# Performance work log

Hardware: AMD Instinct MI355X
Metric: run time of the kernel (lower is better)

Reference implementation:

```python
import jax, jax.numpy as jnp
import numpy as np

HEADS = 16
DIM_HEAD = 64
SCALE = DIM_HEAD ** -0.5
NEG = -jnp.finfo(jnp.float32).max


def setup_inputs() -> dict:
    key = jax.random.key(0)
    k1, k2, k3, k4, k5 = jax.random.split(key, 5)
    dim = 1024
    inner = HEADS * DIM_HEAD
    b, n = 2, 2048
    s = dim ** -0.5
    return {
        "x": jax.random.normal(k1, (b, n, dim), dtype=jnp.float32),
        "Wq": jax.random.normal(k2, (dim, inner), dtype=jnp.float32) * s,
        "Wk": jax.random.normal(k3, (dim, inner), dtype=jnp.float32) * s,
        "Wv": jax.random.normal(k4, (dim, inner), dtype=jnp.float32) * s,
        "Wo": jax.random.normal(k5, (inner, dim), dtype=jnp.float32) * s,
    }


def reference(x, Wq, Wk, Wv, Wo):
    b, n, _ = x.shape
    # project and split heads: b n (h d) -> b h n d
    def split(t):
        return t.reshape(b, n, HEADS, DIM_HEAD).transpose(0, 2, 1, 3)
    q = split(x @ Wq) * SCALE
    k = split(x @ Wk)
    v = split(x @ Wv)
    sim = jnp.einsum('bhid,bhjd->bhij', q, k)
    # causal mask: triu(j - i + 1) masked with -finfo.max
    causal = jnp.triu(jnp.ones((n, n), dtype=bool), k=1)
    sim = jnp.where(causal, NEG, sim)
    attn = jax.nn.softmax(sim, axis=-1)  # dropout p=0.0 -> identity
    out = jnp.einsum('bhij,bhjd->bhid', attn, v)
    out = out.transpose(0, 2, 1, 3).reshape(b, n, HEADS * DIM_HEAD)
    return out @ Wo
```

## Files before the change

### kernel.cpp

```cpp
#include <hip/hip_runtime.h>

#define NHEAD 16
#define DHEAD 64
#define SEQ 2048
#define DMODEL 1024
#define BATCH 2
#define QSCALE 0.1803368801111204f

typedef __bf16 bf16x8 __attribute__((ext_vector_type(8)));
typedef float f32x4 __attribute__((ext_vector_type(4)));
typedef float f32x16 __attribute__((ext_vector_type(16)));
typedef unsigned int u32x4 __attribute__((ext_vector_type(4)));

__device__ inline unsigned short f2bf(float f) {
  unsigned int u = __builtin_bit_cast(unsigned int, f);
  u = (u + 0x7FFFu + ((u >> 16) & 1u)) >> 16;
  return (unsigned short)u;
}

__device__ inline unsigned int cvtpk_bf16(float lo, float hi) {
  unsigned int r;
  asm("v_cvt_pk_bf16_f32 %0, %1, %2" : "=v"(r) : "v"(lo), "v"(hi));
  return r;
}

__device__ inline void pl32swap(unsigned int& a, unsigned int& b) {
  asm volatile("v_permlane32_swap_b32 %0, %1" : "+v"(a), "+v"(b));
}

__global__ __launch_bounds__(256) void k_conv_x(const float* __restrict__ x,
                                                unsigned short* __restrict__ Af) {
  int blk = blockIdx.x;
  int R = blk >> 5, kt = blk & 31;
  int t = threadIdx.x;
  int i = t >> 6, lane = t & 63;
  int n = R * 64 + i * 16 + (lane & 15);
  int k = kt * 32 + (lane >> 4) * 8;
  const float* xp = x + (size_t)n * DMODEL + k;
  float4 v0 = *(const float4*)xp;
  float4 v1 = *(const float4*)(xp + 4);
  ushort4 lo, hi;
  lo.x = f2bf(v0.x); lo.y = f2bf(v0.y); lo.z = f2bf(v0.z); lo.w = f2bf(v0.w);
  hi.x = f2bf(v1.x); hi.y = f2bf(v1.y); hi.z = f2bf(v1.z); hi.w = f2bf(v1.w);
  size_t base = ((size_t)((R * 32 + kt) * 4 + i) * 64 + lane) * 8;
  *(ushort4*)&Af[base] = lo;
  *(ushort4*)&Af[base + 4] = hi;
}

__global__ __launch_bounds__(256) void k_trans_wf(const float* __restrict__ Wq, const float* __restrict__ Wk,
                                                  const float* __restrict__ Wv, const float* __restrict__ Wo,
                                                  unsigned short* __restrict__ Wqf, unsigned short* __restrict__ Wkf,
                                                  unsigned short* __restrict__ Wvf, unsigned short* __restrict__ Wof) {
  __shared__ float ts[32][65];
  int mat = blockIdx.z;
  const float* src = (mat == 0) ? Wq : (mat == 1) ? Wk : (mat == 2) ? Wv : Wo;
  unsigned short* dst = (mat == 0) ? Wqf : (mat == 1) ? Wkf : (mat == 2) ? Wvf : Wof;
  int cb = blockIdx.x, kt = blockIdx.y;
  int t = threadIdx.x;
  int row = t >> 3, seg = t & 7;
  const float* sp = src + (size_t)(kt * 32 + row) * DMODEL + cb * 64 + seg * 8;
  float4 u0 = *(const float4*)sp;
  float4 u1 = *(const float4*)(sp + 4);
  ts[row][seg * 8 + 0] = u0.x; ts[row][seg * 8 + 1] = u0.y;
  ts[row][seg * 8 + 2] = u0.z; ts[row][seg * 8 + 3] = u0.w;
  ts[row][seg * 8 + 4] = u1.x; ts[row][seg * 8 + 5] = u1.y;
  ts[row][seg * 8 + 6] = u1.z; ts[row][seg * 8 + 7] = u1.w;
  __syncthreads();
  int j = t >> 6, lane = t & 63;
  int c_l = j * 16 + (lane & 15);
  int kb = (lane >> 4) * 8;
  ushort4 lo, hi;
  lo.x = f2bf(ts[kb + 0][c_l]); lo.y = f2bf(ts[kb + 1][c_l]);
  lo.z = f2bf(ts[kb + 2][c_l]); lo.w = f2bf(ts[kb + 3][c_l]);
  hi.x = f2bf(ts[kb + 4][c_l]); hi.y = f2bf(ts[kb + 5][c_l]);
  hi.z = f2bf(ts[kb + 6][c_l]); hi.w = f2bf(ts[kb + 7][c_l]);
  size_t base = ((size_t)((cb * 32 + kt) * 4 + j) * 64 + lane) * 8;
  *(ushort4*)&dst[base] = lo;
  *(ushort4*)&dst[base + 4] = hi;
}

__global__ __launch_bounds__(128, 2) void k_gemm_qkv(const unsigned short* __restrict__ Af,
                                                     const unsigned short* __restrict__ Wqf,
                                                     const unsigned short* __restrict__ Wkf,
                                                     const unsigned short* __restrict__ Wvf,
                                                     unsigned short* __restrict__ Qf,
                                                     unsigned short* __restrict__ Kf,
                                                     unsigned short* __restrict__ Vf) {
  int id = blockIdx.x;
  int xcd = id & 7, lid = id >> 3;
  int rq = lid / 12, cw = lid % 12;
  int rho = (xcd >> 1) * 8 + rq;
  int wv = threadIdx.x >> 6;
  int R = rho * 2 + wv;
  int ct = (xcd & 1) * 12 + cw;
  int mat = ct >> 3, cb2 = ct & 7;
  const unsigned short* Bf = (mat == 0) ? Wqf : (mat == 1) ? Wkf : Wvf;
  int lane = threadIdx.x & 63;
  const unsigned short* Ap  = Af + (size_t)R * 65536 + lane * 8;
  const unsigned short* Bp0 = Bf + (size_t)(cb2 * 2) * 65536 + lane * 8;
  const unsigned short* Bp1 = Bp0 + 65536;

  f32x4 acc[4][8] = {};
  bf16x8 a0[4], a1[4], b0[8], b1[8];
#pragma unroll
  for (int i = 0; i < 4; i++) a0[i] = *(const bf16x8*)(Ap + i * 512);
#pragma unroll
  for (int j = 0; j < 4; j++) {
    b0[j]     = *(const bf16x8*)(Bp0 + j * 512);
    b0[4 + j] = *(const bf16x8*)(Bp1 + j * 512);
  }
#pragma unroll 1
  for (int kt = 0; kt < 32; kt += 2) {
    {
      const unsigned short* An = Ap + (kt + 1) * 2048;
      const unsigned short* Bn0 = Bp0 + (kt + 1) * 2048;
      const unsigned short* Bn1 = Bp1 + (kt + 1) * 2048;
#pragma unroll
      for (int i = 0; i < 4; i++) a1[i] = *(const bf16x8*)(An + i * 512);
#pragma unroll
      for (int j = 0; j < 4; j++) {
        b1[j]     = *(const bf16x8*)(Bn0 + j * 512);
        b1[4 + j] = *(const bf16x8*)(Bn1 + j * 512);
      }
    }
#pragma unroll
    for (int i = 0; i < 4; i++)
#pragma unroll
      for (int j = 0; j < 8; j++)
        acc[i][j] = __builtin_amdgcn_mfma_f32_16x16x32_bf16(a0[i], b0[j], acc[i][j], 0, 0, 0);
    if (kt + 2 < 32) {
      const unsigned short* An = Ap + (kt + 2) * 2048;
      const unsigned short* Bn0 = Bp0 + (kt + 2) * 2048;
      const unsigned short* Bn1 = Bp1 + (kt + 2) * 2048;
#pragma unroll
      for (int i = 0; i < 4; i++) a0[i] = *(const bf16x8*)(An + i * 512);
#pragma unroll
      for (int j = 0; j < 4; j++) {
        b0[j]     = *(const bf16x8*)(Bn0 + j * 512);
        b0[4 + j] = *(const bf16x8*)(Bn1 + j * 512);
      }
    }
#pragma unroll
    for (int i = 0; i < 4; i++)
#pragma unroll
      for (int j = 0; j < 8; j++)
        acc[i][j] = __builtin_amdgcn_mfma_f32_16x16x32_bf16(a1[i], b1[j], acc[i][j], 0, 0, 0);
  }

#pragma unroll
  for (int i = 0; i < 4; i++)
#pragma unroll
    for (int j = 0; j < 8; j++) {
      int n_g = R * 64 + i * 16 + ((lane >> 4) << 2);
      int c = cb2 * 128 + j * 16 + (lane & 15);
      int b = n_g >> 11, n0 = n_g & 2047;
      int h = c >> 6, d = c & 63;
      int bh = b * NHEAD + h;
      if (mat == 0) {
        size_t base = ((size_t)(bh * 64 + (n0 >> 5)) * 4 + (d >> 4)) * 512 +
                      (size_t)((((d >> 3) & 1) * 32 + (n0 & 31)) * 8 + (d & 7));
#pragma unroll
        for (int r = 0; r < 4; r++) Qf[base + 8 * r] = f2bf(acc[i][j][r] * QSCALE);
      } else if (mat == 1) {
        size_t base = ((size_t)(bh * 32 + (n0 >> 6)) * 8 + ((d >> 4) + 4 * ((n0 >> 5) & 1))) * 512 +
                      (size_t)((((d >> 3) & 1) * 32 + (n0 & 31)) * 8 + (d & 7));
#pragma unroll
        for (int r = 0; r < 4; r++) Kf[base + 8 * r] = f2bf(acc[i][j][r]);
      } else {
        size_t base = ((size_t)(bh * 32 + (n0 >> 6)) * 8 + (((n0 >> 4) & 3) + 4 * (d >> 5))) * 512 +
                      (size_t)((((n0 >> 3) & 1) * 32 + (d & 31)) * 8 + (n0 & 7));
        ushort4 o;
        o.x = f2bf(acc[i][j][0]); o.y = f2bf(acc[i][j][1]);
        o.z = f2bf(acc[i][j][2]); o.w = f2bf(acc[i][j][3]);
        *(ushort4*)&Vf[base] = o;
      }
    }
}

__global__ __launch_bounds__(64, 2) void k_attn(const unsigned short* __restrict__ Qf,
                                                const unsigned short* __restrict__ Kf,
                                                const unsigned short* __restrict__ Vf,
                                                unsigned short* __restrict__ Obf) {
  int id = blockIdx.x;
  int xcd = id & 7, m = id >> 3;
  int bhl = m & 3, u = m >> 2;
  int bh = xcd * 4 + bhl;
  int v = (u < 32) ? (63 - u) : (u - 32);
  int nk = (v >> 1) + 1;
  int lane = threadIdx.x;
  int h = lane >> 5, ql = lane & 31;
  int qrow = v * 32 + ql;

  const unsigned short* Qp = Qf + (size_t)bh * 131072 + (size_t)v * 2048;
  const unsigned short* Kp = Kf + (size_t)bh * 131072;
  const unsigned short* Vp = Vf + (size_t)bh * 131072;
  int b = bh >> 4, hh = bh & 15;

  bf16x8 qv[4];
#pragma unroll
  for (int ds = 0; ds < 4; ds++)
    qv[ds] = *(const bf16x8*)&Qp[ds * 512 + lane * 8];

  bf16x8 Kr[8], Vr[8];
#pragma unroll
  for (int jj = 0; jj < 8; jj++) Kr[jj] = *(const bf16x8*)&Kp[jj * 512 + lane * 8];
#pragma unroll
  for (int jj = 0; jj < 8; jj++) Vr[jj] = *(const bf16x8*)&Vp[jj * 512 + lane * 8];

  f32x16 o0 = {}, o1 = {};
  float m_r = -3.0e38f, l_r = 0.0f;

#pragma unroll 1
  for (int kc = 0; kc < nk; ++kc) {
    f32x16 s0 = {}, s1 = {};
#pragma unroll
    for (int ds = 0; ds < 4; ds++) {
      s0 = __builtin_amdgcn_mfma_f32_32x32x16_bf16(Kr[ds], qv[ds], s0, 0, 0, 0);
      s1 = __builtin_amdgcn_mfma_f32_32x32x16_bf16(Kr[4 + ds], qv[ds], s1, 0, 0, 0);
    }
    bool pfn = (kc + 1 < nk);
    size_t nb = (size_t)(kc + 1) * 4096;
    if (pfn) {
#pragma unroll
      for (int jj = 0; jj < 8; jj++) Kr[jj] = *(const bf16x8*)&Kp[nb + jj * 512 + lane * 8];
    }
    int k0 = kc * 64;
    if (kc == nk - 1) {
#pragma unroll
      for (int r = 0; r < 16; r++) {
        int kloc = (r & 3) + 8 * (r >> 2) + 4 * h;
        if (k0 + kloc > qrow) s0[r] = -3.0e38f;
        if (k0 + 32 + kloc > qrow) s1[r] = -3.0e38f;
      }
    }
    float t0[8], t1[8];
#pragma unroll
    for (int r = 0; r < 8; r++) t0[r] = fmaxf(s0[r], s0[r + 8]);
#pragma unroll
    for (int r = 0; r < 8; r++) t1[r] = fmaxf(s1[r], s1[r + 8]);
#pragma unroll
    for (int r = 0; r < 4; r++) t0[r] = fmaxf(fmaxf(t0[r], t0[r + 4]), fmaxf(t1[r], t1[r + 4]));
    float pm = fmaxf(fmaxf(t0[0], t0[1]), fmaxf(t0[2], t0[3]));
    pm = fmaxf(pm, __shfl_xor(pm, 32));
    bool grow = pm > m_r + 8.0f;
    float mnew = grow ? pm : m_r;
    float sf = grow ? __builtin_amdgcn_exp2f(m_r - mnew) : 1.0f;
    m_r = mnew;
    float rsum = 0.0f;
#pragma unroll
    for (int r = 0; r < 16; r++) { s0[r] = __builtin_amdgcn_exp2f(s0[r] - m_r); rsum += s0[r]; }
#pragma unroll
    for (int r = 0; r < 16; r++) { s1[r] = __builtin_amdgcn_exp2f(s1[r] - m_r); rsum += s1[r]; }
    l_r = l_r * sf + rsum;
    if (__ballot(grow)) {
#pragma unroll
      for (int r = 0; r < 16; r++) { o0[r] *= sf; o1[r] *= sf; }
    }
    unsigned int pa0 = cvtpk_bf16(s0[0], s0[1]),   pa1 = cvtpk_bf16(s0[2], s0[3]);
    unsigned int pb0 = cvtpk_bf16(s0[4], s0[5]),   pb1 = cvtpk_bf16(s0[6], s0[7]);
    unsigned int pc0 = cvtpk_bf16(s0[8], s0[9]),   pc1 = cvtpk_bf16(s0[10], s0[11]);
    unsigned int pd0 = cvtpk_bf16(s0[12], s0[13]), pd1 = cvtpk_bf16(s0[14], s0[15]);
    unsigned int pe0 = cvtpk_bf16(s1[0], s1[1]),   pe1 = cvtpk_bf16(s1[2], s1[3]);
    unsigned int pf0 = cvtpk_bf16(s1[4], s1[5]),   pf1 = cvtpk_bf16(s1[6], s1[7]);
    unsigned int pg0 = cvtpk_bf16(s1[8], s1[9]),   pg1 = cvtpk_bf16(s1[10], s1[11]);
    unsigned int ph0 = cvtpk_bf16(s1[12], s1[13]), ph1 = cvtpk_bf16(s1[14], s1[15]);
    pl32swap(pa0, pb0); pl32swap(pa1, pb1);
    pl32swap(pc0, pd0); pl32swap(pc1, pd1);
    pl32swap(pe0, pf0); pl32swap(pe1, pf1);
    pl32swap(pg0, ph0); pl32swap(pg1, ph1);
    bf16x8 pfr[4];
    pfr[0] = __builtin_bit_cast(bf16x8, (u32x4){pa0, pa1, pb0, pb1});
    pfr[1] = __builtin_bit_cast(bf16x8, (u32x4){pc0, pc1, pd0, pd1});
    pfr[2] = __builtin_bit_cast(bf16x8, (u32x4){pe0, pe1, pf0, pf1});
    pfr[3] = __builtin_bit_cast(bf16x8, (u32x4){pg0, pg1, ph0, ph1});
#pragma unroll
    for (int ks = 0; ks < 4; ks++) {
      o0 = __builtin_amdgcn_mfma_f32_32x32x16_bf16(Vr[ks], pfr[ks], o0, 0, 0, 0);
      o1 = __builtin_amdgcn_mfma_f32_32x32x16_bf16(Vr[4 + ks], pfr[ks], o1, 0, 0, 0);
    }
    if (pfn) {
#pragma unroll
      for (int jj = 0; jj < 8; jj++) Vr[jj] = *(const bf16x8*)&Vp[nb + jj * 512 + lane * 8];
    }
  }

  float lt = l_r + __shfl_xor(l_r, 32);
  float rl = 1.0f / lt;
  int Rg = b * 32 + (v >> 1);
  int ii = (v * 2 + (ql >> 4)) & 3;
  size_t base0 = ((size_t)(Rg * 32 + 2 * hh) * 4 + ii) * 512 + (size_t)((ql & 15) * 8 + 4 * h);
  size_t base1 = base0 + 2048;
#pragma unroll
  for (int rg = 0; rg < 4; rg++) {
    uint2 w0, w1;
    w0.x = cvtpk_bf16(o0[4 * rg] * rl, o0[4 * rg + 1] * rl);
    w0.y = cvtpk_bf16(o0[4 * rg + 2] * rl, o0[4 * rg + 3] * rl);
    w1.x = cvtpk_bf16(o1[4 * rg] * rl, o1[4 * rg + 1] * rl);
    w1.y = cvtpk_bf16(o1[4 * rg + 2] * rl, o1[4 * rg + 3] * rl);
    *(uint2*)&Obf[base0 + rg * 128] = w0;
    *(uint2*)&Obf[base1 + rg * 128] = w1;
  }
}

__global__ __launch_bounds__(64, 2) void k_gemm_out(const unsigned short* __restrict__ Obf,
                                                    const unsigned short* __restrict__ Wof,
                                                    float* __restrict__ out) {
  int id = blockIdx.x;
  int xcd = id & 7, lid = id >> 3;
  int rg8 = lid >> 4, cb = lid & 15;
  int R = xcd * 8 + rg8;
  int lane = threadIdx.x;
  const unsigned short* Ap = Obf + (size_t)R * 65536 + lane * 8;
  const unsigned short* Bp = Wof + (size_t)cb * 65536 + lane * 8;

  f32x4 acc[4][4] = {};
  bf16x8 a0[4], b0[4], a1[4], b1[4];
#pragma unroll
  for (int i = 0; i < 4; i++) {
    a0[i] = *(const bf16x8*)(Ap + i * 512);
    b0[i] = *(const bf16x8*)(Bp + i * 512);
  }
#pragma unroll 1
  for (int kt = 0; kt < 32; kt += 2) {
    {
      const unsigned short* An = Ap + (kt + 1) * 2048;
      const unsigned short* Bn = Bp + (kt + 1) * 2048;
#pragma unroll
      for (int i = 0; i < 4; i++) {
        a1[i] = *(const bf16x8*)(An + i * 512);
        b1[i] = *(const bf16x8*)(Bn + i * 512);
      }
    }
#pragma unroll
    for (int i = 0; i < 4; i++)
#pragma unroll
      for (int j = 0; j < 4; j++)
        acc[i][j] = __builtin_amdgcn_mfma_f32_16x16x32_bf16(a0[i], b0[j], acc[i][j], 0, 0, 0);
    if (kt + 2 < 32) {
      const unsigned short* An = Ap + (kt + 2) * 2048;
      const unsigned short* Bn = Bp + (kt + 2) * 2048;
#pragma unroll
      for (int i = 0; i < 4; i++) {
        a0[i] = *(const bf16x8*)(An + i * 512);
        b0[i] = *(const bf16x8*)(Bn + i * 512);
      }
    }
#pragma unroll
    for (int i = 0; i < 4; i++)
#pragma unroll
      for (int j = 0; j < 4; j++)
        acc[i][j] = __builtin_amdgcn_mfma_f32_16x16x32_bf16(a1[i], b1[j], acc[i][j], 0, 0, 0);
  }

#pragma unroll
  for (int i = 0; i < 4; i++)
#pragma unroll
    for (int j = 0; j < 4; j++) {
      int n_g = R * 64 + i * 16 + ((lane >> 4) << 2);
      int c = cb * 64 + j * 16 + (lane & 15);
#pragma unroll
      for (int r = 0; r < 4; r++)
        out[(size_t)(n_g + r) * DMODEL + c] = acc[i][j][r];
    }
}

extern "C" void kernel_launch(void* const* d_in, const int* in_sizes, int n_in,
                              void* d_out, int out_size, void* d_ws, size_t ws_size,
                              hipStream_t stream) {
  const float* x  = (const float*)d_in[0];
  const float* Wq = (const float*)d_in[1];
  const float* Wk = (const float*)d_in[2];
  const float* Wv = (const float*)d_in[3];
  const float* Wo = (const float*)d_in[4];
  float* out = (float*)d_out;
  char* ws = (char*)d_ws;
  unsigned short* Af  = (unsigned short*)(ws);
  unsigned short* Wqf = (unsigned short*)(ws + (8ull << 20));
  unsigned short* Wkf = (unsigned short*)(ws + (10ull << 20));
  unsigned short* Wvf = (unsigned short*)(ws + (12ull << 20));
  unsigned short* Wof = (unsigned short*)(ws + (14ull << 20));
  unsigned short* Qf  = (unsigned short*)(ws + (16ull << 20));
  unsigned short* Kf  = (unsigned short*)(ws + (24ull << 20));
  unsigned short* Vf  = (unsigned short*)(ws + (32ull << 20));
  unsigned short* Obf = (unsigned short*)(ws + (40ull << 20));

  k_conv_x<<<dim3(2048), dim3(256), 0, stream>>>(x, Af);
  k_trans_wf<<<dim3(16, 32, 4), dim3(256), 0, stream>>>(Wq, Wk, Wv, Wo, Wqf, Wkf, Wvf, Wof);
  k_gemm_qkv<<<dim3(768), dim3(128), 0, stream>>>(Af, Wqf, Wkf, Wvf, Qf, Kf, Vf);
  k_attn<<<dim3(2048), dim3(64), 0, stream>>>(Qf, Kf, Vf, Obf);
  k_gemm_out<<<dim3(1024), dim3(64), 0, stream>>>(Obf, Wof, out);
}
```

Baseline: 109.8 us.

## Split long causal attention rows into two KV pieces with a merge kernel

Query blocks in the second half of the sequence are split into two work items over key chunks (0-15 and 16+). Each piece writes unnormalized bf16 partial outputs plus per-row max and sum to workspace, and a new merge kernel combines them with log-sum-exp weights. The goal is to balance the causal triangle's uneven work across more, shorter blocks, and occupancy is raised to 3 waves per SIMD. The cost is an extra kernel launch, extra global traffic for the partials, and an added bf16 rounding of intermediate outputs. The partials reuse the workspace regions of Af and Wqf, which are dead by that point.

Result: slower. 113.8 us (+3.6%).

```diff
diff --git a/kernel.cpp b/kernel.cpp
--- a/kernel.cpp
+++ b/kernel.cpp
@@ -27,6 +27,9 @@
 __device__ inline void pl32swap(unsigned int& a, unsigned int& b) {
   asm volatile("v_permlane32_swap_b32 %0, %1" : "+v"(a), "+v"(b));
 }
+
+__device__ inline float bflo(unsigned int u) { return __builtin_bit_cast(float, u << 16); }
+__device__ inline float bfhi(unsigned int u) { return __builtin_bit_cast(float, u & 0xffff0000u); }
 
 __global__ __launch_bounds__(256) void k_conv_x(const float* __restrict__ x,
                                                 unsigned short* __restrict__ Af) {
@@ -177,16 +180,20 @@
     }
 }
 
-__global__ __launch_bounds__(64, 2) void k_attn(const unsigned short* __restrict__ Qf,
-                                                const unsigned short* __restrict__ Kf,
-                                                const unsigned short* __restrict__ Vf,
-                                                unsigned short* __restrict__ Obf) {
+__global__ __launch_bounds__(64, 3) void k_attn_piece(const unsigned short* __restrict__ Qf,
+                                                      const unsigned short* __restrict__ Kf,
+                                                      const unsigned short* __restrict__ Vf,
+                                                      unsigned short* __restrict__ Obf,
+                                                      unsigned int* __restrict__ PartOb,
+                                                      float* __restrict__ PartML) {
   int id = blockIdx.x;
-  int xcd = id & 7, m = id >> 3;
-  int bhl = m & 3, u = m >> 2;
+  int xcd = id & 7, r = id >> 3;
+  int bhl = r / 96, j = r % 96;
   int bh = xcd * 4 + bhl;
-  int v = (u < 32) ? (63 - u) : (u - 32);
-  int nk = (v >> 1) + 1;
+  int v = (j < 64) ? j : 127 - j;
+  int nkFull = (v >> 1) + 1;
+  int c0 = (j < 64) ? 0 : 16;
+  int ce = (j < 64) ? ((nkFull < 16) ? nkFull : 16) : nkFull;
   int lane = threadIdx.x;
   int h = lane >> 5, ql = lane & 31;
   int qrow = v * 32 + ql;
@@ -194,7 +201,6 @@
   const unsigned short* Qp = Qf + (size_t)bh * 131072 + (size_t)v * 2048;
   const unsigned short* Kp = Kf + (size_t)bh * 131072;
   const unsigned short* Vp = Vf + (size_t)bh * 131072;
-  int b = bh >> 4, hh = bh & 15;
 
   bf16x8 qv[4];
 #pragma unroll
@@ -202,44 +208,45 @@
     qv[ds] = *(const bf16x8*)&Qp[ds * 512 + lane * 8];
 
   bf16x8 Kr[8], Vr[8];
-#pragma unroll
-  for (int jj = 0; jj < 8; jj++) Kr[jj] = *(const bf16x8*)&Kp[jj * 512 + lane * 8];
-#pragma unroll
-  for (int jj = 0; jj < 8; jj++) Vr[jj] = *(const bf16x8*)&Vp[jj * 512 + lane * 8];
+  size_t cb0 = (size_t)c0 * 4096;
+#pragma unroll
+  for (int jj = 0; jj < 8; jj++) Kr[jj] = *(const bf16x8*)&Kp[cb0 + jj * 512 + lane * 8];
+#pragma unroll
+  for (int jj = 0; jj < 8; jj++) Vr[jj] = *(const bf16x8*)&Vp[cb0 + jj * 512 + lane * 8];
 
   f32x16 o0 = {}, o1 = {};
   float m_r = -3.0e38f, l_r = 0.0f;
 
 #pragma unroll 1
-  for (int kc = 0; kc < nk; ++kc) {
+  for (int kc = c0; kc < ce; ++kc) {
     f32x16 s0 = {}, s1 = {};
 #pragma unroll
     for (int ds = 0; ds < 4; ds++) {
       s0 = __builtin_amdgcn_mfma_f32_32x32x16_bf16(Kr[ds], qv[ds], s0, 0, 0, 0);
       s1 = __builtin_amdgcn_mfma_f32_32x32x16_bf16(Kr[4 + ds], qv[ds], s1, 0, 0, 0);
     }
-    bool pfn = (kc + 1 < nk);
+    bool pfn = (kc + 1 < ce);
     size_t nb = (size_t)(kc + 1) * 4096;
     if (pfn) {
 #pragma unroll
-      for (int jj = 0; jj < 8; jj++) Kr[jj] = *(const bf16x8*)&Kp[nb + jj * 512 + lane * 8];
+      for (int jj2 = 0; jj2 < 8; jj2++) Kr[jj2] = *(const bf16x8*)&Kp[nb + jj2 * 512 + lane * 8];
     }
     int k0 = kc * 64;
-    if (kc == nk - 1) {
-#pragma unroll
-      for (int r = 0; r < 16; r++) {
-        int kloc = (r & 3) + 8 * (r >> 2) + 4 * h;
-        if (k0 + kloc > qrow) s0[r] = -3.0e38f;
-        if (k0 + 32 + kloc > qrow) s1[r] = -3.0e38f;
+    if (kc == nkFull - 1) {
+#pragma unroll
+      for (int r2 = 0; r2 < 16; r2++) {
+        int kloc = (r2 & 3) + 8 * (r2 >> 2) + 4 * h;
+        if (k0 + kloc > qrow) s0[r2] = -3.0e38f;
+        if (k0 + 32 + kloc > qrow) s1[r2] = -3.0e38f;
       }
     }
     float t0[8], t1[8];
 #pragma unroll
-    for (int r = 0; r < 8; r++) t0[r] = fmaxf(s0[r], s0[r + 8]);
-#pragma unroll
-    for (int r = 0; r < 8; r++) t1[r] = fmaxf(s1[r], s1[r + 8]);
-#pragma unroll
-    for (int r = 0; r < 4; r++) t0[r] = fmaxf(fmaxf(t0[r], t0[r + 4]), fmaxf(t1[r], t1[r + 4]));
+    for (int r2 = 0; r2 < 8; r2++) t0[r2] = fmaxf(s0[r2], s0[r2 + 8]);
+#pragma unroll
+    for (int r2 = 0; r2 < 8; r2++) t1[r2] = fmaxf(s1[r2], s1[r2 + 8]);
+#pragma unroll
+    for (int r2 = 0; r2 < 4; r2++) t0[r2] = fmaxf(fmaxf(t0[r2], t0[r2 + 4]), fmaxf(t1[r2], t1[r2 + 4]));
     float pm = fmaxf(fmaxf(t0[0], t0[1]), fmaxf(t0[2], t0[3]));
     pm = fmaxf(pm, __shfl_xor(pm, 32));
     bool grow = pm > m_r + 8.0f;
@@ -248,13 +255,13 @@
     m_r = mnew;
     float rsum = 0.0f;
 #pragma unroll
-    for (int r = 0; r < 16; r++) { s0[r] = __builtin_amdgcn_exp2f(s0[r] - m_r); rsum += s0[r]; }
-#pragma unroll
-    for (int r = 0; r < 16; r++) { s1[r] = __builtin_amdgcn_exp2f(s1[r] - m_r); rsum += s1[r]; }
+    for (int r2 = 0; r2 < 16; r2++) { s0[r2] = __builtin_amdgcn_exp2f(s0[r2] - m_r); rsum += s0[r2]; }
+#pragma unroll
+    for (int r2 = 0; r2 < 16; r2++) { s1[r2] = __builtin_amdgcn_exp2f(s1[r2] - m_r); rsum += s1[r2]; }
     l_r = l_r * sf + rsum;
     if (__ballot(grow)) {
 #pragma unroll
-      for (int r = 0; r < 16; r++) { o0[r] *= sf; o1[r] *= sf; }
+      for (int r2 = 0; r2 < 16; r2++) { o0[r2] *= sf; o1[r2] *= sf; }
     }
     unsigned int pa0 = cvtpk_bf16(s0[0], s0[1]),   pa1 = cvtpk_bf16(s0[2], s0[3]);
     unsigned int pb0 = cvtpk_bf16(s0[4], s0[5]),   pb1 = cvtpk_bf16(s0[6], s0[7]);
@@ -280,25 +287,81 @@
     }
     if (pfn) {
 #pragma unroll
-      for (int jj = 0; jj < 8; jj++) Vr[jj] = *(const bf16x8*)&Vp[nb + jj * 512 + lane * 8];
+      for (int jj2 = 0; jj2 < 8; jj2++) Vr[jj2] = *(const bf16x8*)&Vp[nb + jj2 * 512 + lane * 8];
     }
   }
 
   float lt = l_r + __shfl_xor(l_r, 32);
-  float rl = 1.0f / lt;
+  if (v < 32) {
+    float rl = 1.0f / lt;
+    int b = bh >> 4, hh = bh & 15;
+    int Rg = b * 32 + (v >> 1);
+    int ii = (v * 2 + (ql >> 4)) & 3;
+    size_t base0 = ((size_t)(Rg * 32 + 2 * hh) * 4 + ii) * 512 + (size_t)((ql & 15) * 8 + 4 * h);
+    size_t base1 = base0 + 2048;
+#pragma unroll
+    for (int rg = 0; rg < 4; rg++) {
+      uint2 w0, w1;
+      w0.x = cvtpk_bf16(o0[4 * rg] * rl, o0[4 * rg + 1] * rl);
+      w0.y = cvtpk_bf16(o0[4 * rg + 2] * rl, o0[4 * rg + 3] * rl);
+      w1.x = cvtpk_bf16(o1[4 * rg] * rl, o1[4 * rg + 1] * rl);
+      w1.y = cvtpk_bf16(o1[4 * rg + 2] * rl, o1[4 * rg + 3] * rl);
+      *(uint2*)&Obf[base0 + rg * 128] = w0;
+      *(uint2*)&Obf[base1 + rg * 128] = w1;
+    }
+  } else {
+    int pidx = (((bh << 5) + (v - 32)) << 1) + ((j >= 64) ? 1 : 0);
+    unsigned int* po = PartOb + (size_t)pidx * 1024 + lane * 16;
+#pragma unroll
+    for (int rg = 0; rg < 4; rg++) {
+      po[rg * 2]     = cvtpk_bf16(o0[4 * rg], o0[4 * rg + 1]);
+      po[rg * 2 + 1] = cvtpk_bf16(o0[4 * rg + 2], o0[4 * rg + 3]);
+      po[8 + rg * 2]     = cvtpk_bf16(o1[4 * rg], o1[4 * rg + 1]);
+      po[8 + rg * 2 + 1] = cvtpk_bf16(o1[4 * rg + 2], o1[4 * rg + 3]);
+    }
+    PartML[(size_t)pidx * 128 + lane * 2]     = m_r;
+    PartML[(size_t)pidx * 128 + lane * 2 + 1] = lt;
+  }
+}
+
+__global__ __launch_bounds__(64, 4) void k_attn_merge(const unsigned int* __restrict__ PartOb,
+                                                      const float* __restrict__ PartML,
+                                                      unsigned short* __restrict__ Obf) {
+  int t = blockIdx.x;
+  int bh = t >> 5, v = 32 + (t & 31);
+  int lane = threadIdx.x, h = lane >> 5, ql = lane & 31;
+  int p0i = ((bh << 5) + (v - 32)) << 1;
+  const unsigned int* q0 = PartOb + (size_t)p0i * 1024 + lane * 16;
+  const unsigned int* q1 = q0 + 1024;
+  float m1 = PartML[(size_t)p0i * 128 + lane * 2];
+  float l1 = PartML[(size_t)p0i * 128 + lane * 2 + 1];
+  float m2 = PartML[(size_t)(p0i + 1) * 128 + lane * 2];
+  float l2 = PartML[(size_t)(p0i + 1) * 128 + lane * 2 + 1];
+  float m = fmaxf(m1, m2);
+  float w1 = __builtin_amdgcn_exp2f(m1 - m);
+  float w2 = __builtin_amdgcn_exp2f(m2 - m);
+  float rl = 1.0f / (w1 * l1 + w2 * l2);
+  float W1 = w1 * rl, W2 = w2 * rl;
+  unsigned int ow[16];
+#pragma unroll
+  for (int w = 0; w < 16; w++) {
+    unsigned int a = q0[w], c = q1[w];
+    float lo = W1 * bflo(a) + W2 * bflo(c);
+    float hi = W1 * bfhi(a) + W2 * bfhi(c);
+    ow[w] = cvtpk_bf16(lo, hi);
+  }
+  int b = bh >> 4, hh = bh & 15;
   int Rg = b * 32 + (v >> 1);
   int ii = (v * 2 + (ql >> 4)) & 3;
   size_t base0 = ((size_t)(Rg * 32 + 2 * hh) * 4 + ii) * 512 + (size_t)((ql & 15) * 8 + 4 * h);
   size_t base1 = base0 + 2048;
 #pragma unroll
   for (int rg = 0; rg < 4; rg++) {
-    uint2 w0, w1;
-    w0.x = cvtpk_bf16(o0[4 * rg] * rl, o0[4 * rg + 1] * rl);
-    w0.y = cvtpk_bf16(o0[4 * rg + 2] * rl, o0[4 * rg + 3] * rl);
-    w1.x = cvtpk_bf16(o1[4 * rg] * rl, o1[4 * rg + 1] * rl);
-    w1.y = cvtpk_bf16(o1[4 * rg + 2] * rl, o1[4 * rg + 3] * rl);
+    uint2 w0, w1u;
+    w0.x  = ow[2 * rg];     w0.y  = ow[2 * rg + 1];
+    w1u.x = ow[8 + 2 * rg]; w1u.y = ow[8 + 2 * rg + 1];
     *(uint2*)&Obf[base0 + rg * 128] = w0;
-    *(uint2*)&Obf[base1 + rg * 128] = w1;
+    *(uint2*)&Obf[base1 + rg * 128] = w1u;
   }
 }
 
@@ -383,10 +446,13 @@
   unsigned short* Kf  = (unsigned short*)(ws + (24ull << 20));
   unsigned short* Vf  = (unsigned short*)(ws + (32ull << 20));
   unsigned short* Obf = (unsigned short*)(ws + (40ull << 20));
+  unsigned int* PartOb = (unsigned int*)(ws);
+  float* PartML = (float*)(ws + (8ull << 20));
 
   k_conv_x<<<dim3(2048), dim3(256), 0, stream>>>(x, Af);
   k_trans_wf<<<dim3(16, 32, 4), dim3(256), 0, stream>>>(Wq, Wk, Wv, Wo, Wqf, Wkf, Wvf, Wof);
   k_gemm_qkv<<<dim3(768), dim3(128), 0, stream>>>(Af, Wqf, Wkf, Wvf, Qf, Kf, Vf);
-  k_attn<<<dim3(2048), dim3(64), 0, stream>>>(Qf, Kf, Vf, Obf);
+  k_attn_piece<<<dim3(3072), dim3(64), 0, stream>>>(Qf, Kf, Vf, Obf, PartOb, PartML);
+  k_attn_merge<<<dim3(1024), dim3(64), 0, stream>>>(PartOb, PartML, Obf);
   k_gemm_out<<<dim3(1024), dim3(64), 0, stream>>>(Obf, Wof, out);
 }
```
